# Kernel tuning notes

Hardware: AMD Instinct MI355X
Metric: run time of the kernel (lower is better)

The kernel has to match this reference:

```python
import jax, jax.numpy as jnp
import numpy as np

H, W, S, B = 256, 256, 16, 8  # dim=(H,W); S hardcoded in forward; B = 1 + events[-1,-1]
N = 4_000_000


def _shift2d(a, dy, dx):
    """Replicates F.pad(a, (pad(dx) + pad(dy)))[:H,:W] where pad(n)=(n,0) if n>=0 else (0,-n).
    Positive diff shifts content right/down and zero-fills; negative diff is a no-op
    (right/bottom padding followed by top-left crop is identity)."""
    sy = jnp.maximum(dy, 0)
    sx = jnp.maximum(dx, 0)
    a = jnp.roll(a, shift=(sy, sx), axis=(0, 1))
    row = jnp.arange(a.shape[0])[:, None]
    col = jnp.arange(a.shape[1])[None, :]
    return jnp.where((row >= sy) & (col >= sx), a, 0.0)


def setup_inputs():
    key = jax.random.key(0)
    k1, k2, k3, k4 = jax.random.split(key, 4)
    x = jax.random.randint(k1, (N,), 0, W).astype(jnp.float32)
    y = jax.random.randint(k2, (N,), 0, H).astype(jnp.float32)
    t = jax.random.uniform(k3, (N,), minval=1e-3, maxval=1.0)
    p = (jax.random.randint(k4, (N,), 0, 2) * 2 - 1).astype(jnp.float32)
    b = jnp.repeat(jnp.arange(B, dtype=jnp.float32), N // B)  # sorted so events[-1,-1]==B-1
    events = jnp.stack([x, y, t, p, b], axis=1)
    return {"events": events}


def _forward(events):
    x = events[:, 0]
    y = events[:, 1]
    t = events[:, 2]
    bi = events[:, 4].astype(jnp.int32)

    # per-batch time normalization: t /= max(t) within each sample
    t_max = jax.ops.segment_max(t, bi, num_segments=B)
    t = t / t_max[bi]

    xi = x.astype(jnp.int32)
    yi = y.astype(jnp.int32)

    # container: per-pixel event count histogram, (B,H,W)
    idx_c = xi + W * yi + W * H * bi
    container = jnp.zeros(B * H * W, jnp.int32).at[idx_c].add(1).reshape(B, H, W)

    # time_segment[e] = number of thresholds i/S (i=1..S-1) with t >= i/S
    thr = jnp.arange(1, S, dtype=t.dtype) / S
    ts = jnp.searchsorted(thr, t, side='right').astype(jnp.int32)

    # combiner accumulates the segment index itself (as in the torch code)
    idx_cb = xi + W * yi + W * H * ts + W * H * S * bi
    combiner = jnp.zeros(B * S * H * W, jnp.int32).at[idx_cb].add(ts)
    combiner = combiner.reshape(B, S, H, W).astype(jnp.float32)

    # per-(batch, segment) event counts and x/y centroids
    seg = bi * S + ts
    cnt = jax.ops.segment_sum(jnp.ones_like(t), seg, num_segments=B * S).reshape(B, S)
    xm = jax.ops.segment_sum(x, seg, num_segments=B * S).reshape(B, S) / cnt
    ym = jax.ops.segment_sum(y, seg, num_segments=B * S).reshape(B, S) / cnt

    # mean-shift alignment + accumulation of the S segment images
    combined = []
    for b_ in range(B):
        segment = combiner[b_, 0]
        x_mean = xm[b_, 0]
        y_mean = ym[b_, 0]
        pts = cnt[b_, 0]  # note: never updated in the original code
        for i in range(1, S):
            cond = cnt[b_, i] > pts
            tmp = jnp.where(cond, segment, combiner[b_, i])
            base = jnp.where(cond, combiner[b_, i], segment)
            dx = jnp.floor(jnp.where(cond, xm[b_, i] - x_mean, x_mean - xm[b_, i])).astype(jnp.int32)
            dy = jnp.floor(jnp.where(cond, ym[b_, i] - y_mean, y_mean - ym[b_, i])).astype(jnp.int32)
            x_mean = jnp.where(cond, xm[b_, i], x_mean)
            y_mean = jnp.where(cond, ym[b_, i], y_mean)
            segment = base + _shift2d(tmp, dy, dx)
        combined.append(jax.nn.relu(segment - S))
    combined_img = jnp.stack(combined)  # (B,H,W)

    # half-resolution count + mean-timestamp voxel grids
    hw4 = (H // 2) * (W // 2)
    idx_ct = xi // 2 + (W // 2) * (yi // 2) + (W * H * bi) // 4
    counter = jnp.zeros(B * hw4, jnp.int32).at[idx_ct].add(1).astype(jnp.float32)
    divider = jnp.where(counter == 0, 1.0, counter)
    timer = jnp.zeros(B * hw4, jnp.float32).at[idx_ct].add(t) / divider
    counter = counter.reshape(B, H // 2, W // 2)
    timer = timer.reshape(B, H // 2, W // 2)

    # 2x2 difference pooling of the count image
    dyv = container[:, ::2] - container[:, 1::2]
    dyv = (dyv[:, :, ::2] + dyv[:, :, 1::2]).astype(jnp.float32)
    dxv = container[:, :, ::2] - container[:, :, 1::2]
    dxv = (dxv[:, 1::2] + dxv[:, ::2]).astype(jnp.float32)

    # F.interpolate(scale_factor=0.5, mode='nearest') == ::2 subsampling for even H,W
    combined_half = combined_img[:, ::2, ::2]

    return jnp.stack([dxv, dyv, timer, counter, combined_half], axis=1)  # (B,5,H/2,W/2)


def reference(events):
    return _forward(events)
```

## Files before the change

kernel.cpp:

```cpp
#include <hip/hip_runtime.h>

#define SS 16
#define BB 8
#define CHUNKS 32

#define OFF_CNT    0
#define OFF_XS     512
#define OFF_YS     1024
#define OFF_BMAX   1536
#define OFF_P4REP  (1536 + 4096)
#define OFF_CMREP  (1536 + 4096 + 16777216)
#define OFF_REC    (1536 + 4096 + 16777216 + 8388608)


__global__ void k_tmax(const float4* __restrict__ ev4, int nq, unsigned* __restrict__ bmax,
                       int* __restrict__ cnt, int* __restrict__ xs, int* __restrict__ ys) {
    if (blockIdx.x == 0 && threadIdx.x < BB * SS) {
        cnt[threadIdx.x] = 0; xs[threadIdx.x] = 0; ys[threadIdx.x] = 0;
    }
    int bb = blockIdx.x >> 7;
    long base = (long)bb * nq;
    unsigned m = 0;
    for (int q = (blockIdx.x & 127) * blockDim.x + threadIdx.x; q < nq; q += 128 * blockDim.x) {
        const float4* p = ev4 + (base + q) * 5;
        float4 f0 = p[0], f1 = p[1], f3 = p[3], f4 = p[4];
        unsigned t0 = __float_as_uint(f0.z), t1 = __float_as_uint(f1.w);
        unsigned t2 = __float_as_uint(f3.x), t3 = __float_as_uint(f4.y);
        unsigned a = t0 > t1 ? t0 : t1;
        unsigned b2 = t2 > t3 ? t2 : t3;
        a = a > b2 ? a : b2;
        m = m > a ? m : a;
    }
    #pragma unroll
    for (int off = 32; off; off >>= 1) {
        unsigned o = (unsigned)__shfl_xor((int)m, off, 64);
        m = m > o ? m : o;
    }
    __shared__ unsigned sm;
    if (threadIdx.x == 0) sm = 0;
    __syncthreads();
    if ((threadIdx.x & 63) == 0) atomicMax(&sm, m);
    __syncthreads();
    if (threadIdx.x == 0) bmax[blockIdx.x] = sm;
}

__global__ void __launch_bounds__(1024, 8)
k_main(const float4* __restrict__ ev4, int nq,
       const unsigned* __restrict__ bmax,
       unsigned* __restrict__ p4rep, uint4* __restrict__ rec4,
       int* __restrict__ cnt, int* __restrict__ xs, int* __restrict__ ys) {
    __shared__ unsigned p4s[16384];
    __shared__ unsigned long long stat[SS * 8];
    __shared__ unsigned stmax;
    int bb = blockIdx.x >> 5;
    int ch = blockIdx.x & 31;
    if (threadIdx.x == 0) stmax = 0u;
    if (threadIdx.x < SS * 8) stat[threadIdx.x] = 0ull;
    for (int i = threadIdx.x; i < 16384; i += 1024) p4s[i] = 0u;
    __syncthreads();
    if (threadIdx.x < 128) atomicMax(&stmax, bmax[bb * 128 + threadIdx.x]);
    __syncthreads();
    float tm = __uint_as_float(stmax);
    long base = (long)bb * nq;
    int slot = threadIdx.x & 7;
    for (int q = ch * 1024 + threadIdx.x; q < nq; q += CHUNKS * 1024) {
        const float4* p = ev4 + (base + q) * 5;
        float4 f0 = p[0], f1 = p[1], f2 = p[2], f3 = p[3], f4 = p[4];
        float X[4] = { f0.x, f1.y, f2.z, f3.w };
        float Y[4] = { f0.y, f1.z, f2.w, f4.x };
        float T[4] = { f0.z, f1.w, f3.x, f4.y };
        unsigned r[4];
        #pragma unroll
        for (int k = 0; k < 4; k++) {
            int xi = (int)X[k], yi = (int)Y[k];
            float tn = __fdiv_rn(T[k], tm);
            int ts = (int)(tn * 16.0f);
            if (ts > 15) ts = 15;
            unsigned qfix = __float2uint_rn(tn * 256.0f);
            unsigned v = qfix | (1u << 14)
                | (((unsigned)(xi & 1) ^ 1u) << 20)
                | (((unsigned)(yi & 1) ^ 1u) << 26);
            atomicAdd(&p4s[((yi >> 1) << 7) + (xi >> 1)], v);
            atomicAdd(&stat[ts * 8 + slot], 1ull | ((unsigned long long)xi << 20)
                                                 | ((unsigned long long)yi << 42));
            r[k] = (unsigned)xi | ((unsigned)yi << 8) | ((unsigned)ts << 16);
        }
        rec4[base + q] = make_uint4(r[0], r[1], r[2], r[3]);
    }
    __syncthreads();
    unsigned* dst = p4rep + (long)blockIdx.x * 16384;
    for (int i = threadIdx.x; i < 16384; i += 1024) dst[i] = p4s[i];
    if (threadIdx.x < SS) {
        unsigned long long v = 0ull;
        #pragma unroll
        for (int s = 0; s < 8; s++) v += stat[threadIdx.x * 8 + s];
        if (v) {
            int g = bb * SS + threadIdx.x;
            atomicAdd(&cnt[g], (int)(v & 0xFFFFF));
            atomicAdd(&xs[g],  (int)((v >> 20) & 0x3FFFFF));
            atomicAdd(&ys[g],  (int)(v >> 42));
        }
    }
}

__global__ void __launch_bounds__(1024, 8)
k_comb(const uint4* __restrict__ rec4, int nq,
       const int* __restrict__ cnt, const int* __restrict__ xs, const int* __restrict__ ys,
       const unsigned* __restrict__ p4rep,
       unsigned* __restrict__ cmrep32, float* __restrict__ out) {
    __shared__ int combs[16384];
    __shared__ double xm[SS], ym[SS];
    __shared__ int cs[SS], ssy[SS], ssx[SS];
    int bb = blockIdx.x >> 5;
    int ch = blockIdx.x & 31;
    for (int i = threadIdx.x; i < 16384; i += 1024) combs[i] = 0;
    if (threadIdx.x < SS) {
        int g = bb * SS + threadIdx.x;
        int cc = cnt[g];
        cs[threadIdx.x] = cc;
        xm[threadIdx.x] = (double)xs[g] / (double)cc;
        ym[threadIdx.x] = (double)ys[g] / (double)cc;
    }
    __syncthreads();
    if (threadIdx.x == 0) {
        double x_mean = xm[0], y_mean = ym[0];
        int c0 = cs[0];
        int sy[SS], sx[SS];
        for (int k = 0; k < SS; k++) { sy[k] = 0; sx[k] = 0; }
        for (int k = 1; k < SS; k++) {
            bool cond = cs[k] > c0;
            double ddx = cond ? (xm[k] - x_mean) : (x_mean - xm[k]);
            double ddy = cond ? (ym[k] - y_mean) : (y_mean - ym[k]);
            int dx = (int)floor(ddx);
            int dy = (int)floor(ddy);
            int px = dx > 0 ? dx : 0;
            int py = dy > 0 ? dy : 0;
            if (cond) {
                for (int j = 0; j < k; j++) { sy[j] += py; sx[j] += px; }
                x_mean = xm[k]; y_mean = ym[k];
            } else {
                sy[k] = py; sx[k] = px;
            }
        }
        for (int k = 0; k < SS; k++) { ssy[k] = sy[k]; ssx[k] = sx[k]; }
    }
    __syncthreads();
    long base = (long)bb * nq;
    for (int q = ch * 1024 + threadIdx.x; q < nq; q += CHUNKS * 1024) {
        uint4 rv = rec4[base + q];
        unsigned R[4] = { rv.x, rv.y, rv.z, rv.w };
        #pragma unroll
        for (int k = 0; k < 4; k++) {
            unsigned r = R[k];
            int ts = r >> 16;
            if (ts) {
                int yy = ((r >> 8) & 255) + ssy[ts];
                int xx = (r & 255) + ssx[ts];
                if (yy < 256 && xx < 256 && !((yy | xx) & 1))
                    atomicAdd(&combs[((yy >> 1) << 7) + (xx >> 1)], ts);
            }
        }
    }
    __syncthreads();
    unsigned* dst = cmrep32 + (long)blockIdx.x * 8192;
    for (int i = threadIdx.x; i < 8192; i += 1024)
        dst[i] = (unsigned)combs[2 * i] | ((unsigned)combs[2 * i + 1] << 16);
    if (threadIdx.x < 512) {
        int lin = blockIdx.x * 512 + threadIdx.x;
        int hp = lin & 16383;
        int b  = lin >> 14;
        long rb = (long)b * CHUNKS * 16384 + hp;
        unsigned tfix = 0; int c = 0, Ex = 0, Ey = 0;
        #pragma unroll 8
        for (int r = 0; r < CHUNKS; r++) {
            unsigned v = p4rep[rb + (long)r * 16384];
            tfix += v & 0x3FFFu;
            c    += (int)((v >> 14) & 63u);
            Ex   += (int)((v >> 20) & 63u);
            Ey   += (int)(v >> 26);
        }
        float tsum = (float)tfix * (1.0f / 256.0f);
        float ctr = (float)c;
        int obase = (b * 5) << 14;
        out[obase             + hp] = (float)(2 * Ex - c);
        out[obase +     16384 + hp] = (float)(2 * Ey - c);
        out[obase + 2 * 16384 + hp] = tsum / (c == 0 ? 1.0f : ctr);
        out[obase + 3 * 16384 + hp] = ctr;
    }
}

__global__ void k_out(const unsigned short* __restrict__ cmrep,
                      float* __restrict__ out) {
    int lin = blockIdx.x * blockDim.x + threadIdx.x;
    int hp = lin & 16383;
    int b  = lin >> 14;
    long rb = (long)b * CHUNKS * 16384 + hp;
    int cm = 0;
    #pragma unroll 8
    for (int r = 0; r < CHUNKS; r++) cm += cmrep[rb + (long)r * 16384];
    float cmb = (float)cm - 16.0f;
    cmb = cmb < 0.0f ? 0.0f : cmb;
    out[((b * 5 + 4) << 14) + hp] = cmb;
}

extern "C" void kernel_launch(void* const* d_in, const int* in_sizes, int n_in,
                              void* d_out, int out_size, void* d_ws, size_t ws_size,
                              hipStream_t stream) {
    const float4* ev4 = (const float4*)d_in[0];
    int n  = in_sizes[0] / 5;
    int nb = n / BB;
    int nq = nb / 4;
    char* ws = (char*)d_ws;
    int*      cnt  = (int*)     (ws + OFF_CNT);
    int*      xs   = (int*)     (ws + OFF_XS);
    int*      ys   = (int*)     (ws + OFF_YS);
    unsigned* bmax = (unsigned*)(ws + OFF_BMAX);
    unsigned* p4rep = (unsigned*)(ws + OFF_P4REP);
    unsigned* cmrep32 = (unsigned*)(ws + OFF_CMREP);
    uint4*    rec4  = (uint4*)  (ws + OFF_REC);

    hipLaunchKernelGGL(k_tmax, dim3(1024), dim3(256),  0, stream, ev4, nq, bmax,
                       cnt, xs, ys);
    hipLaunchKernelGGL(k_main, dim3(256),  dim3(1024), 0, stream, ev4, nq, bmax,
                       p4rep, rec4, cnt, xs, ys);
    hipLaunchKernelGGL(k_comb, dim3(256),  dim3(1024), 0, stream, rec4, nq,
                       cnt, xs, ys, p4rep, cmrep32, (float*)d_out);
    hipLaunchKernelGGL(k_out,  dim3(128),  dim3(1024), 0, stream,
                       (const unsigned short*)cmrep32, (float*)d_out);
}
```

Before: 143.7 us.

## Compact event coordinates and timestamps in prep pass to cut later reads

The first pass now also writes packed 8-bit x/y coordinates and a contiguous timestamp array while computing per-batch max time. The main and combiner kernels read these compact arrays instead of re-reading the 20-byte-per-event input and a 16-byte record. The segment index is stored as 4-bit nibbles in a 2-byte record. This is meant to reduce total global memory traffic, at the cost of extra writes in the first pass and narrower, less efficient 2-byte accesses.

```diff
diff --git a/kernel.cpp b/kernel.cpp
--- a/kernel.cpp
+++ b/kernel.cpp
@@ -8,12 +8,15 @@
 #define OFF_XS     512
 #define OFF_YS     1024
 #define OFF_BMAX   1536
-#define OFF_P4REP  (1536 + 4096)
-#define OFF_CMREP  (1536 + 4096 + 16777216)
-#define OFF_REC    (1536 + 4096 + 16777216 + 8388608)
-
-
-__global__ void k_tmax(const float4* __restrict__ ev4, int nq, unsigned* __restrict__ bmax,
+#define OFF_P4REP  5632
+#define OFF_CMREP  (5632 + 16777216)
+#define OFF_XYREC  (5632 + 16777216 + 8388608)
+#define OFF_TARR   (5632 + 16777216 + 8388608 + 8000000)
+#define OFF_TSREC  (5632 + 16777216 + 8388608 + 8000000 + 16000000)
+
+
+__global__ void k_prep(const float4* __restrict__ ev4, int nq, unsigned* __restrict__ bmax,
+                       uint2* __restrict__ xyrec, float4* __restrict__ tarr,
                        int* __restrict__ cnt, int* __restrict__ xs, int* __restrict__ ys) {
     if (blockIdx.x == 0 && threadIdx.x < BB * SS) {
         cnt[threadIdx.x] = 0; xs[threadIdx.x] = 0; ys[threadIdx.x] = 0;
@@ -23,7 +26,13 @@
     unsigned m = 0;
     for (int q = (blockIdx.x & 127) * blockDim.x + threadIdx.x; q < nq; q += 128 * blockDim.x) {
         const float4* p = ev4 + (base + q) * 5;
-        float4 f0 = p[0], f1 = p[1], f3 = p[3], f4 = p[4];
+        float4 f0 = p[0], f1 = p[1], f2 = p[2], f3 = p[3], f4 = p[4];
+        unsigned xy0 = (unsigned)(int)f0.x | ((unsigned)(int)f0.y << 8)
+                     | ((unsigned)(int)f1.y << 16) | ((unsigned)(int)f1.z << 24);
+        unsigned xy1 = (unsigned)(int)f2.z | ((unsigned)(int)f2.w << 8)
+                     | ((unsigned)(int)f3.w << 16) | ((unsigned)(int)f4.x << 24);
+        xyrec[base + q] = make_uint2(xy0, xy1);
+        tarr[base + q]  = make_float4(f0.z, f1.w, f3.x, f4.y);
         unsigned t0 = __float_as_uint(f0.z), t1 = __float_as_uint(f1.w);
         unsigned t2 = __float_as_uint(f3.x), t3 = __float_as_uint(f4.y);
         unsigned a = t0 > t1 ? t0 : t1;
@@ -45,9 +54,9 @@
 }
 
 __global__ void __launch_bounds__(1024, 8)
-k_main(const float4* __restrict__ ev4, int nq,
+k_main(const uint2* __restrict__ xyrec, const float4* __restrict__ tarr, int nq,
        const unsigned* __restrict__ bmax,
-       unsigned* __restrict__ p4rep, uint4* __restrict__ rec4,
+       unsigned* __restrict__ p4rep, unsigned short* __restrict__ tsrec,
        int* __restrict__ cnt, int* __restrict__ xs, int* __restrict__ ys) {
     __shared__ unsigned p4s[16384];
     __shared__ unsigned long long stat[SS * 8];
@@ -64,15 +73,14 @@
     long base = (long)bb * nq;
     int slot = threadIdx.x & 7;
     for (int q = ch * 1024 + threadIdx.x; q < nq; q += CHUNKS * 1024) {
-        const float4* p = ev4 + (base + q) * 5;
-        float4 f0 = p[0], f1 = p[1], f2 = p[2], f3 = p[3], f4 = p[4];
-        float X[4] = { f0.x, f1.y, f2.z, f3.w };
-        float Y[4] = { f0.y, f1.z, f2.w, f4.x };
-        float T[4] = { f0.z, f1.w, f3.x, f4.y };
-        unsigned r[4];
+        uint2 xy = xyrec[base + q];
+        float4 t4 = tarr[base + q];
+        float T[4] = { t4.x, t4.y, t4.z, t4.w };
+        unsigned XY[4] = { xy.x & 0xFFFFu, xy.x >> 16, xy.y & 0xFFFFu, xy.y >> 16 };
+        unsigned tsn = 0;
         #pragma unroll
         for (int k = 0; k < 4; k++) {
-            int xi = (int)X[k], yi = (int)Y[k];
+            int xi = (int)(XY[k] & 255u), yi = (int)(XY[k] >> 8);
             float tn = __fdiv_rn(T[k], tm);
             int ts = (int)(tn * 16.0f);
             if (ts > 15) ts = 15;
@@ -83,9 +91,9 @@
             atomicAdd(&p4s[((yi >> 1) << 7) + (xi >> 1)], v);
             atomicAdd(&stat[ts * 8 + slot], 1ull | ((unsigned long long)xi << 20)
                                                  | ((unsigned long long)yi << 42));
-            r[k] = (unsigned)xi | ((unsigned)yi << 8) | ((unsigned)ts << 16);
-        }
-        rec4[base + q] = make_uint4(r[0], r[1], r[2], r[3]);
+            tsn |= (unsigned)ts << (4 * k);
+        }
+        tsrec[base + q] = (unsigned short)tsn;
     }
     __syncthreads();
     unsigned* dst = p4rep + (long)blockIdx.x * 16384;
@@ -104,7 +112,7 @@
 }
 
 __global__ void __launch_bounds__(1024, 8)
-k_comb(const uint4* __restrict__ rec4, int nq,
+k_comb(const uint2* __restrict__ xyrec, const unsigned short* __restrict__ tsrec, int nq,
        const int* __restrict__ cnt, const int* __restrict__ xs, const int* __restrict__ ys,
        const unsigned* __restrict__ p4rep,
        unsigned* __restrict__ cmrep32, float* __restrict__ out) {
@@ -147,15 +155,15 @@
     __syncthreads();
     long base = (long)bb * nq;
     for (int q = ch * 1024 + threadIdx.x; q < nq; q += CHUNKS * 1024) {
-        uint4 rv = rec4[base + q];
-        unsigned R[4] = { rv.x, rv.y, rv.z, rv.w };
+        uint2 xy = xyrec[base + q];
+        unsigned tsn = tsrec[base + q];
+        unsigned XY[4] = { xy.x & 0xFFFFu, xy.x >> 16, xy.y & 0xFFFFu, xy.y >> 16 };
         #pragma unroll
         for (int k = 0; k < 4; k++) {
-            unsigned r = R[k];
-            int ts = r >> 16;
+            int ts = (int)((tsn >> (4 * k)) & 15u);
             if (ts) {
-                int yy = ((r >> 8) & 255) + ssy[ts];
-                int xx = (r & 255) + ssx[ts];
+                int yy = (int)(XY[k] >> 8) + ssy[ts];
+                int xx = (int)(XY[k] & 255u) + ssx[ts];
                 if (yy < 256 && xx < 256 && !((yy | xx) & 1))
                     atomicAdd(&combs[((yy >> 1) << 7) + (xx >> 1)], ts);
             }
@@ -211,19 +219,21 @@
     int nb = n / BB;
     int nq = nb / 4;
     char* ws = (char*)d_ws;
-    int*      cnt  = (int*)     (ws + OFF_CNT);
-    int*      xs   = (int*)     (ws + OFF_XS);
-    int*      ys   = (int*)     (ws + OFF_YS);
-    unsigned* bmax = (unsigned*)(ws + OFF_BMAX);
+    int*      cnt   = (int*)     (ws + OFF_CNT);
+    int*      xs    = (int*)     (ws + OFF_XS);
+    int*      ys    = (int*)     (ws + OFF_YS);
+    unsigned* bmax  = (unsigned*)(ws + OFF_BMAX);
     unsigned* p4rep = (unsigned*)(ws + OFF_P4REP);
     unsigned* cmrep32 = (unsigned*)(ws + OFF_CMREP);
-    uint4*    rec4  = (uint4*)  (ws + OFF_REC);
-
-    hipLaunchKernelGGL(k_tmax, dim3(1024), dim3(256),  0, stream, ev4, nq, bmax,
-                       cnt, xs, ys);
-    hipLaunchKernelGGL(k_main, dim3(256),  dim3(1024), 0, stream, ev4, nq, bmax,
-                       p4rep, rec4, cnt, xs, ys);
-    hipLaunchKernelGGL(k_comb, dim3(256),  dim3(1024), 0, stream, rec4, nq,
+    uint2*    xyrec = (uint2*)   (ws + OFF_XYREC);
+    float4*   tarr  = (float4*)  (ws + OFF_TARR);
+    unsigned short* tsrec = (unsigned short*)(ws + OFF_TSREC);
+
+    hipLaunchKernelGGL(k_prep, dim3(1024), dim3(256),  0, stream, ev4, nq, bmax,
+                       xyrec, tarr, cnt, xs, ys);
+    hipLaunchKernelGGL(k_main, dim3(256),  dim3(1024), 0, stream, xyrec, tarr, nq,
+                       bmax, p4rep, tsrec, cnt, xs, ys);
+    hipLaunchKernelGGL(k_comb, dim3(256),  dim3(1024), 0, stream, xyrec, tsrec, nq,
                        cnt, xs, ys, p4rep, cmrep32, (float*)d_out);
     hipLaunchKernelGGL(k_out,  dim3(128),  dim3(1024), 0, stream,
                        (const unsigned short*)cmrep32, (float*)d_out);
```

After: 137.4 us (median of 2 runs). 1.05x faster.
